# Optimization experiments

Measured on AMD Instinct MI355X. Metric: run time of the kernel, lower is better.

The kernel has to match this reference:

```python
import jax, jax.numpy as jnp
import numpy as np

B, TGT, SRC, H = 32, 512, 2048, 512


def setup_inputs() -> dict:
    key = jax.random.key(0)
    k1, k2, k3, k4, k5 = jax.random.split(key, 5)
    s = 1.0 / np.sqrt(H)
    return {
        "decoder_output": jax.random.normal(k1, (B, TGT, H), jnp.float32),
        "encoder_outputs": jax.random.normal(k2, (B, SRC, H), jnp.float32),
        # lengths in [SRC//2, SRC] so every row has at least one valid position
        "encoder_inputs_length": jax.random.randint(k3, (B,), SRC // 2, SRC + 1, jnp.int64),
        "W_in": jax.random.normal(k4, (H, H), jnp.float32) * s,   # linear_in weight (general)
        "W_out": jax.random.normal(k5, (H, 2 * H), jnp.float32) * s,  # linear_out weight, no bias
    }


def reference(decoder_output, encoder_outputs, encoder_inputs_length, W_in, W_out):
    # score (general): (q @ W_in^T) @ enc^T -> [B, tgt, src]
    q = jnp.einsum('bth,oh->bto', decoder_output, W_in)
    align = jnp.einsum('bth,bsh->bts', q, encoder_outputs)
    # mask positions j >= length with -inf, then softmax over src dim
    mask = jnp.arange(SRC)[None, None, :] < encoder_inputs_length[:, None, None]  # [B,1,src]
    align = jnp.where(mask, align, -jnp.inf)
    align_vectors = jax.nn.softmax(align, axis=2)  # [B, tgt, src]
    # context: [B, tgt, H]
    context = jnp.einsum('bts,bsh->bth', align_vectors, encoder_outputs)
    concat = jnp.concatenate([context, decoder_output], axis=2)  # [B, tgt, 2H]
    attn_h = jnp.tanh(jnp.einsum('btk,ok->bto', concat, W_out))  # [B, tgt, H]
    # transpose to [tgt, B, ...] as the torch module does
    return attn_h.transpose(1, 0, 2), align_vectors.transpose(1, 0, 2)
```

## Files before the change

### kernel.cpp

```cpp
#include <hip/hip_runtime.h>

#define Bc   32
#define TGTc 512
#define SRCc 2048
#define Hc   512

typedef unsigned short u16;
typedef unsigned int   u32;
typedef __attribute__((ext_vector_type(8))) short s16x8;
typedef __attribute__((ext_vector_type(4))) float f32x4;
typedef __attribute__((ext_vector_type(4))) unsigned short u16x4;

__device__ __forceinline__ u16 f2bf(float x) {
    u32 u = __float_as_uint(x);
    u32 r = (u + 0x7FFFu + ((u >> 16) & 1u)) >> 16;
    return (u16)r;
}
__device__ __forceinline__ float bf2f(u16 h) {
    return __uint_as_float(((u32)h) << 16);
}


__global__ void prep_len_k(const u32* __restrict__ raw, int* __restrict__ out) {
    int i = threadIdx.x;
    if (i >= Bc) return;
    bool is64 = (raw[1] == 0u);
    out[i] = (int)(is64 ? raw[2 * i] : raw[i]);
}

__global__ __launch_bounds__(256) void split_k(const float* __restrict__ in,
                                               u16* __restrict__ hi, u16* __restrict__ lo,
                                               int n4) {
    int stride = gridDim.x * 256;
    for (int i = blockIdx.x * 256 + threadIdx.x; i < n4; i += stride) {
        f32x4 x = ((const f32x4*)in)[i];
        u16x4 h, l;
#pragma unroll
        for (int j = 0; j < 4; j++) {
            u16 hb = f2bf(x[j]);
            h[j] = hb;
            l[j] = f2bf(x[j] - bf2f(hb));
        }
        ((u16x4*)hi)[i] = h;
        ((u16x4*)lo)[i] = l;
    }
}

__global__ __launch_bounds__(256) void split_wout_k(const float* __restrict__ in,
                                                    u16* __restrict__ ah, u16* __restrict__ al,
                                                    u16* __restrict__ bh, u16* __restrict__ bl) {
    int i = blockIdx.x * 256 + threadIdx.x;
    if (i >= 512 * 256) return;
    int o = i >> 8, kc = i & 255;
    f32x4 x = ((const f32x4*)in)[i];
    u16x4 h, l;
#pragma unroll
    for (int j = 0; j < 4; j++) {
        u16 hb = f2bf(x[j]);
        h[j] = hb;
        l[j] = f2bf(x[j] - bf2f(hb));
    }
    int half = kc >> 7;
    int idx = o * 128 + (kc & 127);
    ((u16x4*)(half ? bh : ah))[idx] = h;
    ((u16x4*)(half ? bl : al))[idx] = l;
}

__global__ __launch_bounds__(256) void prep_enc_k(const float* __restrict__ enc,
                                                  u16* __restrict__ ehi, u16* __restrict__ elo,
                                                  u16* __restrict__ ethi) {
    __shared__ float tile[32][33];
    const int b = blockIdx.z;
    const int s0 = blockIdx.x << 5, h0 = blockIdx.y << 5;
    const int x = threadIdx.x & 31, y = threadIdx.x >> 5;
    const long base = ((long)b * SRCc + s0) * Hc + h0;
#pragma unroll
    for (int j = 0; j < 4; j++) {
        int s = (y << 2) + j;
        float v = enc[base + (long)s * Hc + x];
        tile[s][x] = v;
        u16 h = f2bf(v);
        long o = base + (long)s * Hc + x;
        ehi[o] = h;
        elo[o] = f2bf(v - bf2f(h));
    }
    __syncthreads();
    const long tbase = ((long)b * Hc + h0) * SRCc + s0;
#pragma unroll
    for (int j = 0; j < 4; j++) {
        int hh = (y << 2) + j;
        float v = tile[x][hh];
        long o = tbase + (long)hh * SRCc + x;
        ethi[o] = f2bf(v);
    }
}


struct GArgs {
    const u16* A0; const u16* A1;
    const u16* B0; const u16* B1;
    const u16* A2; const u16* A3;
    const u16* B2; const u16* B3;
    void* out0; void* out1;
};

__device__ __forceinline__ void gload_lds16(const u16* g, u16* l) {
    __builtin_amdgcn_global_load_lds((const __attribute__((address_space(1))) void*)g,
                                     (__attribute__((address_space(3))) void*)l, 16, 0, 0);
}

template <int CFG>
__global__ __launch_bounds__(256, 3) void gemm_bt(GArgs g) {
    constexpr int NA = (CFG == 2) ? 1 : 2;
    constexpr int NB = (CFG == 2) ? 1 : 2;
    constexpr int NC = (CFG == 2) ? 1 : 3;
    constexpr int K  = (CFG == 2) ? 2048 : (CFG == 3 ? 1024 : 512);
    constexpr int KST = (CFG == 3) ? 512 : K;
    constexpr int NT = NA + NB;

    __shared__ u16 lds[NT * 128 * 32];

    const int tid = threadIdx.x;
    const int lane = tid & 63;
    const int wave = tid >> 6;
    const int wm = wave >> 1;
    const int wn = wave & 1;

    int bz = 0, mt, nt;
    if constexpr (CFG == 1 || CFG == 2) { bz = blockIdx.z; mt = blockIdx.y; nt = blockIdx.x; }
    else { mt = blockIdx.x; nt = blockIdx.y; }

    const u16* apt[2][2];
    const u16* bpt[2][2];
    if constexpr (CFG == 1) {
        const long ao = (long)bz * TGTc * Hc, bo = (long)bz * SRCc * Hc;
        apt[0][0] = g.A0 + ao; apt[0][1] = g.A1 + ao;
        bpt[0][0] = g.B0 + bo; bpt[0][1] = g.B1 + bo;
    } else if constexpr (CFG == 2) {
        apt[0][0] = g.A0 + (long)bz * TGTc * SRCc;
        bpt[0][0] = g.B0 + (long)bz * Hc * SRCc;
    } else if constexpr (CFG == 3) {
        apt[0][0] = g.A0; apt[0][1] = g.A1; apt[1][0] = g.A2; apt[1][1] = g.A3;
        bpt[0][0] = g.B0; bpt[0][1] = g.B1; bpt[1][0] = g.B2; bpt[1][1] = g.B3;
    } else {
        apt[0][0] = g.A0; apt[0][1] = g.A1;
        bpt[0][0] = g.B0; bpt[0][1] = g.B1;
    }

    f32x4 acc[4][4];
#pragma unroll
    for (int mi = 0; mi < 4; mi++)
#pragma unroll
        for (int ni = 0; ni < 4; ni++)
            acc[mi][ni] = (f32x4){0.f, 0.f, 0.f, 0.f};

    const int arow0 = mt * 128;
    const int brow0 = nt * 128;

    constexpr int cAi[3] = {0, 0, 1};
    constexpr int cBi[3] = {0, 1, 0};

    const int csw = (((lane >> 4) ^ (lane & 3)) << 3);

    for (int k0 = 0; k0 < K; k0 += 32) {
        int sel = 0, kk = k0;
        if constexpr (CFG == 3) { sel = k0 >> 9; kk = k0 & 511; }
#pragma unroll
        for (int t = 0; t < NT; t++) {
            const u16* base = (t < NA) ? (apt[sel][t] + (long)arow0 * KST + kk)
                                       : (bpt[sel][t - NA] + (long)brow0 * KST + kk);
            u16* dstbase = &lds[t * 4096];
#pragma unroll
            for (int it = 0; it < 2; ++it) {
                int l = it * 256 + tid;
                int row = l >> 2;
                int kel = ((l & 3) ^ (row & 3)) << 3;
                gload_lds16(base + (long)row * KST + kel, dstbase + it * 2048 + wave * 512);
            }
        }
        __syncthreads();

        s16x8 af[NA][4];
        s16x8 bfr[NB][4];
#pragma unroll
        for (int i = 0; i < NA; i++)
#pragma unroll
            for (int f = 0; f < 4; f++) {
                int r = wm * 64 + f * 16 + (lane & 15);
                af[i][f] = *(const s16x8*)&lds[i * 4096 + r * 32 + csw];
            }
#pragma unroll
        for (int i = 0; i < NB; i++)
#pragma unroll
            for (int f = 0; f < 4; f++) {
                int r = wn * 64 + f * 16 + (lane & 15);
                bfr[i][f] = *(const s16x8*)&lds[(NA + i) * 4096 + r * 32 + csw];
            }

#pragma unroll
        for (int c = 0; c < NC; c++)
#pragma unroll
            for (int mi = 0; mi < 4; mi++)
#pragma unroll
                for (int ni = 0; ni < 4; ni++)
                    acc[mi][ni] = __builtin_amdgcn_mfma_f32_16x16x32_bf16(
                        af[cAi[c]][mi], bfr[cBi[c]][ni], acc[mi][ni], 0, 0, 0);
        __syncthreads();
    }

    const int m0 = mt * 128 + wm * 64;
    const int n0 = nt * 128 + wn * 64;
    const int ln15 = lane & 15;
    const int rg = (lane >> 4) << 2;

#pragma unroll
    for (int mi = 0; mi < 4; mi++) {
#pragma unroll
        for (int ni = 0; ni < 4; ni++) {
            f32x4 v = acc[mi][ni];
            int n = n0 + ni * 16 + ln15;
#pragma unroll
            for (int j = 0; j < 4; j++) {
                int m = m0 + mi * 16 + rg + j;
                float x = v[j];
                if constexpr (CFG == 0) {
                    long idx = (long)m * Hc + n;
                    u16 h = f2bf(x);
                    ((u16*)g.out0)[idx] = h;
                    ((u16*)g.out1)[idx] = f2bf(x - bf2f(h));
                } else if constexpr (CFG == 1) {
                    ((float*)g.out0)[((long)m * Bc + bz) * SRCc + n] = x;
                } else if constexpr (CFG == 2) {
                    long idx = ((long)bz * TGTc + m) * Hc + n;
                    u16 h = f2bf(x);
                    ((u16*)g.out0)[idx] = h;
                    ((u16*)g.out1)[idx] = f2bf(x - bf2f(h));
                } else {
                    float th = tanhf(x);
                    int t = m & (TGTc - 1), b = m >> 9;
                    ((float*)g.out0)[((long)t * Bc + b) * Hc + n] = th;
                }
            }
        }
    }
}

__global__ __launch_bounds__(256) void softmax_k(float* __restrict__ align, u16* __restrict__ Pb,
                                                 const int* __restrict__ lens) {
    const int row = blockIdx.x;
    const int b = row >> 9, t = row & (TGTc - 1);
    float* p = align + ((long)t * Bc + b) * SRCc;
    u16* pb = Pb + ((long)b * TGTc + t) * SRCc;
    const int len = lens[b];
    const int tid = threadIdx.x;

    f32x4 v[2];
    float mx = -3.4e38f;
#pragma unroll
    for (int i = 0; i < 2; i++) {
        int s0 = i * 1024 + tid * 4;
        v[i] = *(const f32x4*)&p[s0];
#pragma unroll
        for (int j = 0; j < 4; j++) {
            if (s0 + j >= len) v[i][j] = -3.4e38f;
            mx = fmaxf(mx, v[i][j]);
        }
    }
#pragma unroll
    for (int o = 32; o >= 1; o >>= 1) mx = fmaxf(mx, __shfl_xor(mx, o));
    __shared__ float red[8];
    if ((tid & 63) == 0) red[tid >> 6] = mx;
    __syncthreads();
    mx = fmaxf(fmaxf(red[0], red[1]), fmaxf(red[2], red[3]));

    float sum = 0.f;
    f32x4 e[2];
#pragma unroll
    for (int i = 0; i < 2; i++) {
        int s0 = i * 1024 + tid * 4;
#pragma unroll
        for (int j = 0; j < 4; j++) {
            float ev = (s0 + j >= len) ? 0.f : __expf(v[i][j] - mx);
            e[i][j] = ev;
            sum += ev;
        }
    }
#pragma unroll
    for (int o = 32; o >= 1; o >>= 1) sum += __shfl_xor(sum, o);
    if ((tid & 63) == 0) red[4 + (tid >> 6)] = sum;
    __syncthreads();
    sum = (red[4] + red[5]) + (red[6] + red[7]);
    float inv = 1.f / sum;

#pragma unroll
    for (int i = 0; i < 2; i++) {
        int s0 = i * 1024 + tid * 4;
        f32x4 o4;
        u16x4 h4;
#pragma unroll
        for (int j = 0; j < 4; j++) {
            float pv = e[i][j] * inv;
            o4[j] = pv;
            h4[j] = f2bf(pv);
        }
        *(f32x4*)&p[s0] = o4;
        *(u16x4*)&pb[s0] = h4;
    }
}


extern "C" void kernel_launch(void* const* d_in, const int* in_sizes, int n_in,
                              void* d_out, int out_size, void* d_ws, size_t ws_size,
                              hipStream_t stream) {
    const float* dec  = (const float*)d_in[0];
    const float* enc  = (const float*)d_in[1];
    const u32*   lenp = (const u32*)d_in[2];
    const float* win  = (const float*)d_in[3];
    const float* wout = (const float*)d_in[4];

    float* out_attn  = (float*)d_out;
    float* out_align = out_attn + (size_t)TGTc * Bc * Hc;

    char* w = (char*)d_ws;
    auto take = [&](size_t n) { char* p = w; w += (n + 255) & ~(size_t)255; return p; };
    int* lens      = (int*)take(256);
    u16* dec_hi    = (u16*)take((size_t)8388608 * 2);
    u16* dec_lo    = (u16*)take((size_t)8388608 * 2);
    u16* win_hi    = (u16*)take((size_t)262144 * 2);
    u16* win_lo    = (u16*)take((size_t)262144 * 2);
    u16* wA_hi     = (u16*)take((size_t)262144 * 2);
    u16* wA_lo     = (u16*)take((size_t)262144 * 2);
    u16* wB_hi     = (u16*)take((size_t)262144 * 2);
    u16* wB_lo     = (u16*)take((size_t)262144 * 2);
    u16* enc_hi    = (u16*)take((size_t)33554432 * 2);
    u16* enc_lo    = (u16*)take((size_t)33554432 * 2);
    u16* encT_hi   = (u16*)take((size_t)33554432 * 2);
    u16* q_hi   = (u16*)out_attn;
    u16* q_lo   = q_hi + 8388608;
    u16* Pb     = enc_hi;
    u16* ctx_hi = enc_lo;
    u16* ctx_lo = enc_lo + 8388608;
    (void)in_sizes; (void)n_in; (void)out_size; (void)ws_size;

    prep_len_k<<<1, 64, 0, stream>>>(lenp, lens);
    split_k<<<2048, 256, 0, stream>>>(dec, dec_hi, dec_lo, 8388608 / 4);
    split_k<<<256, 256, 0, stream>>>(win, win_hi, win_lo, 262144 / 4);
    split_wout_k<<<512, 256, 0, stream>>>(wout, wA_hi, wA_lo, wB_hi, wB_lo);
    prep_enc_k<<<dim3(64, 16, 32), 256, 0, stream>>>(enc, enc_hi, enc_lo, encT_hi);

    GArgs a1 = {};
    a1.A0 = dec_hi; a1.A1 = dec_lo; a1.B0 = win_hi; a1.B1 = win_lo;
    a1.out0 = q_hi; a1.out1 = q_lo;
    gemm_bt<0><<<dim3(128, 4, 1), 256, 0, stream>>>(a1);

    GArgs a2 = {};
    a2.A0 = q_hi; a2.A1 = q_lo; a2.B0 = enc_hi; a2.B1 = enc_lo;
    a2.out0 = out_align;
    gemm_bt<1><<<dim3(16, 4, 32), 256, 0, stream>>>(a2);

    softmax_k<<<16384, 256, 0, stream>>>(out_align, Pb, lens);

    GArgs a4 = {};
    a4.A0 = Pb; a4.B0 = encT_hi;
    a4.out0 = ctx_hi; a4.out1 = ctx_lo;
    gemm_bt<2><<<dim3(4, 4, 32), 256, 0, stream>>>(a4);

    GArgs a5 = {};
    a5.A0 = ctx_hi; a5.A1 = ctx_lo; a5.B0 = wA_hi; a5.B1 = wA_lo;
    a5.A2 = dec_hi; a5.A3 = dec_lo; a5.B2 = wB_hi; a5.B3 = wB_lo;
    a5.out0 = out_attn;
    gemm_bt<3><<<dim3(128, 4, 1), 256, 0, stream>>>(a5);
}
```

Baseline: 671.8 us.

## Vectorize encoder prep transpose, merge weight split kernels, drop LDS swizzle

Replaces the encoder prep kernel with a 64x64-tile version that loads float4 and stores 4-wide bf16 vectors for the hi, lo and transposed outputs, cutting scalar global traffic. Merges the W_in and W_out split kernels into one launch to save a launch. Removes the XOR swizzle on the GEMM LDS tile layout, which saves index arithmetic but may bring back LDS bank conflicts on the fragment reads.

```diff
diff --git a/kernel.cpp b/kernel.cpp
--- a/kernel.cpp
+++ b/kernel.cpp
@@ -46,52 +46,82 @@
     }
 }
 
-__global__ __launch_bounds__(256) void split_wout_k(const float* __restrict__ in,
-                                                    u16* __restrict__ ah, u16* __restrict__ al,
-                                                    u16* __restrict__ bh, u16* __restrict__ bl) {
-    int i = blockIdx.x * 256 + threadIdx.x;
-    if (i >= 512 * 256) return;
-    int o = i >> 8, kc = i & 255;
-    f32x4 x = ((const f32x4*)in)[i];
-    u16x4 h, l;
+__global__ __launch_bounds__(256) void split_weights_k(const float* __restrict__ win,
+                                                       const float* __restrict__ wout,
+                                                       u16* __restrict__ wih, u16* __restrict__ wil,
+                                                       u16* __restrict__ ah, u16* __restrict__ al,
+                                                       u16* __restrict__ bh, u16* __restrict__ bl) {
+    int blk = blockIdx.x;
+    if (blk < 256) {
+        int i = blk * 256 + threadIdx.x;
+        f32x4 x = ((const f32x4*)win)[i];
+        u16x4 h, l;
+#pragma unroll
+        for (int j = 0; j < 4; j++) {
+            u16 hb = f2bf(x[j]);
+            h[j] = hb;
+            l[j] = f2bf(x[j] - bf2f(hb));
+        }
+        ((u16x4*)wih)[i] = h;
+        ((u16x4*)wil)[i] = l;
+    } else {
+        int i = (blk - 256) * 256 + threadIdx.x;
+        int o = i >> 8, kc = i & 255;
+        f32x4 x = ((const f32x4*)wout)[i];
+        u16x4 h, l;
+#pragma unroll
+        for (int j = 0; j < 4; j++) {
+            u16 hb = f2bf(x[j]);
+            h[j] = hb;
+            l[j] = f2bf(x[j] - bf2f(hb));
+        }
+        int half = kc >> 7;
+        int idx = o * 128 + (kc & 127);
+        ((u16x4*)(half ? bh : ah))[idx] = h;
+        ((u16x4*)(half ? bl : al))[idx] = l;
+    }
+}
+
+__global__ __launch_bounds__(256) void prep_enc_v2(const float* __restrict__ enc,
+                                                   u16* __restrict__ ehi, u16* __restrict__ elo,
+                                                   u16* __restrict__ ethi) {
+    __shared__ float tile[64][67];
+    const int b = blockIdx.z;
+    const int s0 = blockIdx.x << 6, h0 = blockIdx.y << 6;
+    const int t = threadIdx.x;
+    const int si = t >> 4;
+    const int h4 = (t & 15) << 2;
+    const long base = ((long)b * SRCc + s0) * Hc + h0;
 #pragma unroll
     for (int j = 0; j < 4; j++) {
-        u16 hb = f2bf(x[j]);
-        h[j] = hb;
-        l[j] = f2bf(x[j] - bf2f(hb));
-    }
-    int half = kc >> 7;
-    int idx = o * 128 + (kc & 127);
-    ((u16x4*)(half ? bh : ah))[idx] = h;
-    ((u16x4*)(half ? bl : al))[idx] = l;
-}
-
-__global__ __launch_bounds__(256) void prep_enc_k(const float* __restrict__ enc,
-                                                  u16* __restrict__ ehi, u16* __restrict__ elo,
-                                                  u16* __restrict__ ethi) {
-    __shared__ float tile[32][33];
-    const int b = blockIdx.z;
-    const int s0 = blockIdx.x << 5, h0 = blockIdx.y << 5;
-    const int x = threadIdx.x & 31, y = threadIdx.x >> 5;
-    const long base = ((long)b * SRCc + s0) * Hc + h0;
+        int s = si + j * 16;
+        long o = base + (long)s * Hc + h4;
+        f32x4 v = *(const f32x4*)&enc[o];
+        tile[s][h4 + 0] = v[0];
+        tile[s][h4 + 1] = v[1];
+        tile[s][h4 + 2] = v[2];
+        tile[s][h4 + 3] = v[3];
+        u16x4 hh, ll;
+#pragma unroll
+        for (int k = 0; k < 4; k++) {
+            u16 hb = f2bf(v[k]);
+            hh[k] = hb;
+            ll[k] = f2bf(v[k] - bf2f(hb));
+        }
+        ((u16x4*)ehi)[o >> 2] = hh;
+        ((u16x4*)elo)[o >> 2] = ll;
+    }
+    __syncthreads();
+    const int hi_ = t >> 4;
+    const int s4 = (t & 15) << 2;
+    const long tbase = ((long)b * Hc + h0) * SRCc + s0;
 #pragma unroll
     for (int j = 0; j < 4; j++) {
-        int s = (y << 2) + j;
-        float v = enc[base + (long)s * Hc + x];
-        tile[s][x] = v;
-        u16 h = f2bf(v);
-        long o = base + (long)s * Hc + x;
-        ehi[o] = h;
-        elo[o] = f2bf(v - bf2f(h));
-    }
-    __syncthreads();
-    const long tbase = ((long)b * Hc + h0) * SRCc + s0;
-#pragma unroll
-    for (int j = 0; j < 4; j++) {
-        int hh = (y << 2) + j;
-        float v = tile[x][hh];
-        long o = tbase + (long)hh * SRCc + x;
-        ethi[o] = f2bf(v);
+        int h = hi_ + j * 16;
+        u16x4 hh;
+#pragma unroll
+        for (int k = 0; k < 4; k++) hh[k] = f2bf(tile[s4 + k][h]);
+        ((u16x4*)ethi)[(tbase + (long)h * SRCc + s4) >> 2] = hh;
     }
 }
 
@@ -160,8 +190,6 @@
     constexpr int cAi[3] = {0, 0, 1};
     constexpr int cBi[3] = {0, 1, 0};
 
-    const int csw = (((lane >> 4) ^ (lane & 3)) << 3);
-
     for (int k0 = 0; k0 < K; k0 += 32) {
         int sel = 0, kk = k0;
         if constexpr (CFG == 3) { sel = k0 >> 9; kk = k0 & 511; }
@@ -174,7 +202,7 @@
             for (int it = 0; it < 2; ++it) {
                 int l = it * 256 + tid;
                 int row = l >> 2;
-                int kel = ((l & 3) ^ (row & 3)) << 3;
+                int kel = (l & 3) << 3;
                 gload_lds16(base + (long)row * KST + kel, dstbase + it * 2048 + wave * 512);
             }
         }
@@ -187,14 +215,14 @@
 #pragma unroll
             for (int f = 0; f < 4; f++) {
                 int r = wm * 64 + f * 16 + (lane & 15);
-                af[i][f] = *(const s16x8*)&lds[i * 4096 + r * 32 + csw];
+                af[i][f] = *(const s16x8*)&lds[i * 4096 + r * 32 + ((lane >> 4) << 3)];
             }
 #pragma unroll
         for (int i = 0; i < NB; i++)
 #pragma unroll
             for (int f = 0; f < 4; f++) {
                 int r = wn * 64 + f * 16 + (lane & 15);
-                bfr[i][f] = *(const s16x8*)&lds[(NA + i) * 4096 + r * 32 + csw];
+                bfr[i][f] = *(const s16x8*)&lds[(NA + i) * 4096 + r * 32 + ((lane >> 4) << 3)];
             }
 
 #pragma unroll
@@ -344,9 +372,9 @@
 
     prep_len_k<<<1, 64, 0, stream>>>(lenp, lens);
     split_k<<<2048, 256, 0, stream>>>(dec, dec_hi, dec_lo, 8388608 / 4);
-    split_k<<<256, 256, 0, stream>>>(win, win_hi, win_lo, 262144 / 4);
-    split_wout_k<<<512, 256, 0, stream>>>(wout, wA_hi, wA_lo, wB_hi, wB_lo);
-    prep_enc_k<<<dim3(64, 16, 32), 256, 0, stream>>>(enc, enc_hi, enc_lo, encT_hi);
+    split_weights_k<<<768, 256, 0, stream>>>(win, wout, win_hi, win_lo,
+                                             wA_hi, wA_lo, wB_hi, wB_lo);
+    prep_enc_v2<<<dim3(32, 8, 32), 256, 0, stream>>>(enc, enc_hi, enc_lo, encT_hi);
 
     GArgs a1 = {};
     a1.A0 = dec_hi; a1.A1 = dec_lo; a1.B0 = win_hi; a1.B1 = win_lo;
```

After: 650.3 us. 3.2% less time.
